# Performance work log

Measured on AMD Instinct MI355X. Metric: run time of the kernel, lower is better.

The kernel has to match this reference:

```python
import jax, jax.numpy as jnp
import numpy as np

B = 64        # graphs per batch
N0 = 131072   # total nodes (2048 per graph)
E = 1048576   # total edges (within-graph)
H = 128       # hidden_size
C = 7         # class_num (input feature dim)
EPS = 1e-5


def setup_inputs() -> dict:
    key = jax.random.key(0)
    ks = jax.random.split(key, 16)
    n0 = N0 // B
    x = jax.random.normal(ks[0], (N0, C), dtype=jnp.float32)
    # within-graph random edges: edge e belongs to graph e // (E//B)
    g = jnp.repeat(jnp.arange(B, dtype=jnp.int32), E // B)
    row = jax.random.randint(ks[1], (E,), 0, n0, dtype=jnp.int32) + g * n0
    col = jax.random.randint(ks[2], (E,), 0, n0, dtype=jnp.int32) + g * n0
    edge_index = jnp.stack([row, col], axis=0)
    batch = jnp.repeat(jnp.arange(B, dtype=jnp.int32), n0)
    s = 0.05
    params = dict(
        Wc1=jax.random.normal(ks[3], (C, H), jnp.float32) * s,     # conv1 weight
        Wc=jax.random.normal(ks[4], (3, H, H), jnp.float32) * s,   # conv2-4 weights
        bc=jax.random.normal(ks[5], (4, H), jnp.float32) * s,      # conv biases
        Wf=jax.random.normal(ks[6], (4, H, H), jnp.float32) * s,   # fc weights
        bf=jax.random.normal(ks[7], (4, H), jnp.float32) * s,      # fc biases
        bn_g=jnp.ones((4, H), jnp.float32),                        # BN gamma
        bn_b=jnp.zeros((4, H), jnp.float32),                       # BN beta
        Ws1=jax.random.normal(ks[8], (4, H, 1), jnp.float32) * s,  # SAG GraphConv root weight
        Ws2=jax.random.normal(ks[9], (4, H, 1), jnp.float32) * s,  # SAG GraphConv neighbor weight
        bs=jax.random.normal(ks[10], (4, 1), jnp.float32) * s,     # SAG GraphConv bias
    )
    return dict(x=x, edge_index=edge_index, batch=batch, **params)


def _gcn_conv(x, W, b, row, col, m, N):
    # PyG GCNConv with self loops: out_i = sum_{j->i} h_j / sqrt(d_i d_j) + h_i / d_i + b
    h = x @ W
    deg = jax.ops.segment_sum(m, col, num_segments=N) + 1.0  # +1 for self loop
    dis = jax.lax.rsqrt(deg)
    norm = dis[row] * dis[col] * m  # masked-out edges contribute 0
    agg = jax.ops.segment_sum(h[row] * norm[:, None], col, num_segments=N)
    return agg + h * (dis * dis)[:, None] + b


def _sag_score(x, W1, W2, b, row, col, m, N):
    # GraphConv(H, 1, aggr='add'): score_i = W1^T x_i + W2^T sum_{j->i} x_j + b
    nbr = jax.ops.segment_sum(x[row] * m[:, None], col, num_segments=N)
    return (x @ W1 + nbr @ W2 + b).reshape(-1)


def _bn(x, g, b):
    mu = jnp.mean(x, axis=0)
    var = jnp.mean((x - mu) ** 2, axis=0)  # biased, matches torch BN training
    return (x - mu) * jax.lax.rsqrt(var + EPS) * g + b


def reference(x, edge_index, batch, Wc1, Wc, bc, Wf, bf, bn_g, bn_b, Ws1, Ws2, bs):
    row, col = edge_index[0], edge_index[1]
    m = jnp.ones(row.shape, x.dtype)  # edge validity mask (static-size edge list)
    n = x.shape[0] // B               # nodes per graph (equal-size graphs)
    for i in range(4):
        N = B * n
        W = Wc1 if i == 0 else Wc[i - 1]
        h = _gcn_conv(x, W, bc[i], row, col, m, N)
        h = jax.nn.relu(h @ Wf[i] + bf[i])
        h = _bn(h, bn_g[i], bn_b[i])
        # SAGPooling(ratio=0.5): per-graph top-k by GraphConv score, x *= tanh(score)
        score = _sag_score(h, Ws1[i], Ws2[i], bs[i], row, col, m, N)
        k = n // 2
        _, idx = jax.lax.top_k(score.reshape(B, n), k)  # [B, k] per-graph indices
        perm = (idx + jnp.arange(B, dtype=idx.dtype)[:, None] * n).reshape(-1)
        x = h[perm] * jnp.tanh(score[perm])[:, None]
        # re-index edges; mask edges touching removed nodes
        inv = jnp.full((N,), -1, dtype=row.dtype).at[perm].set(
            jnp.arange(B * k, dtype=row.dtype))
        nr, nc = inv[row], inv[col]
        valid = (nr >= 0) & (nc >= 0)
        m = m * valid.astype(m.dtype)
        row = jnp.where(valid, nr, 0)
        col = jnp.where(valid, nc, 0)
        n = k
    # global_mean_pool over block-structured batch -> [B, H]
    return x.reshape(B, n, -1).mean(axis=1)
```

## Files before the change

### kernel.cpp

```cpp
#include <hip/hip_runtime.h>
#include <cstdint>

#define HB 128
#define NB 64
#define NE 1048576
#define EG (NE / 256)

typedef float v2f __attribute__((ext_vector_type(2)));

__global__ __launch_bounds__(256) void init_edges_k(const int* __restrict__ ei,
    int* __restrict__ row, int* __restrict__ col, int* __restrict__ gcnt0,
    int* __restrict__ ecnt0, int E) {
  int e = blockIdx.x * blockDim.x + threadIdx.x;
  if (e < E) { row[e] = ei[e]; col[e] = ei[E + e]; }
  if (blockIdx.x == 0) {
    if (threadIdx.x < NB) gcnt0[threadIdx.x] = E / NB;
    if (threadIdx.x == 0) *ecnt0 = E;
  }
}

__global__ __launch_bounds__(256) void conv_fc0_k(const float* __restrict__ aggx,
    const float* __restrict__ Wc1, const float* __restrict__ bc0,
    const float* __restrict__ Wf, const float* __restrict__ bf0,
    float* __restrict__ out, int N, float* __restrict__ stat) {
  __shared__ float lt[64][128];
  __shared__ float laggx[64][8];
  __shared__ float lwc1[7 * 128];
  float2 (*red)[128] = (float2(*)[128])lt;
  int tid = threadIdx.x;
  int tx = tid & 31, ty = tid >> 5;
  long rowbase = (long)blockIdx.x * 64;
  for (int i = tid; i < 7 * 32; i += 256)
    ((float4*)lwc1)[i] = ((const float4*)Wc1)[i];
  if (tid < 128) {
    int lr = tid >> 1, lq = (tid & 1) * 4;
    *(float4*)&laggx[lr][lq] = *(const float4*)(aggx + (rowbase + lr) * 8 + lq);
  }
  __syncthreads();
  float4 tacc[8];
  float4 bcv = ((const float4*)bc0)[tx];
  #pragma unroll
  for (int r = 0; r < 8; ++r) tacc[r] = bcv;
  #pragma unroll
  for (int k = 0; k < 7; ++k) {
    float4 wv = ((float4*)lwc1)[k * 32 + tx];
    #pragma unroll
    for (int r = 0; r < 8; ++r) {
      float xv = laggx[ty + 8 * r][k];
      tacc[r].x += xv * wv.x; tacc[r].y += xv * wv.y;
      tacc[r].z += xv * wv.z; tacc[r].w += xv * wv.w;
    }
  }
  #pragma unroll
  for (int r = 0; r < 8; ++r)
    *(float4*)&lt[ty + 8 * r][4 * tx] = tacc[r];
  __syncthreads();
  v2f acc2[16];
  #pragma unroll
  for (int r = 0; r < 16; ++r) acc2[r] = (v2f){0.f, 0.f};
  for (int kc = 0; kc < 16; ++kc) {
    float4 wreg[8];
    #pragma unroll
    for (int k = 0; k < 8; ++k)
      wreg[k] = *(const float4*)(Wf + (size_t)(kc * 8 + k) * HB + 4 * tx);
    #pragma unroll
    for (int kk = 0; kk < 8; kk += 4) {
      float4 xreg[8];
      #pragma unroll
      for (int r = 0; r < 8; ++r)
        xreg[r] = *(const float4*)&lt[ty + 8 * r][kc * 8 + kk];
      #pragma unroll
      for (int k2 = 0; k2 < 4; ++k2) {
        float4 wv = wreg[kk + k2];
        v2f wlo = {wv.x, wv.y}, whi = {wv.z, wv.w};
        #pragma unroll
        for (int r = 0; r < 8; ++r) {
          float xv = ((const float*)&xreg[r])[k2];
          v2f xvv = {xv, xv};
          acc2[2 * r]     += xvv * wlo;
          acc2[2 * r + 1] += xvv * whi;
        }
      }
    }
  }
  float4 bv = ((const float4*)bf0)[tx];
  float4 psum = make_float4(0.f, 0.f, 0.f, 0.f);
  float4 psq  = make_float4(0.f, 0.f, 0.f, 0.f);
  __syncthreads();
  #pragma unroll
  for (int r = 0; r < 8; ++r) {
    float4 v;
    v.x = fmaxf(acc2[2 * r].x + bv.x, 0.f);
    v.y = fmaxf(acc2[2 * r].y + bv.y, 0.f);
    v.z = fmaxf(acc2[2 * r + 1].x + bv.z, 0.f);
    v.w = fmaxf(acc2[2 * r + 1].y + bv.w, 0.f);
    psum.x += v.x; psum.y += v.y; psum.z += v.z; psum.w += v.w;
    psq.x += v.x * v.x; psq.y += v.y * v.y;
    psq.z += v.z * v.z; psq.w += v.w * v.w;
    *(float4*)(out + (size_t)(rowbase + ty + 8 * r) * HB + 4 * tx) = v;
  }
  red[ty][4 * tx + 0] = make_float2(psum.x, psq.x);
  red[ty][4 * tx + 1] = make_float2(psum.y, psq.y);
  red[ty][4 * tx + 2] = make_float2(psum.z, psq.z);
  red[ty][4 * tx + 3] = make_float2(psum.w, psq.w);
  __syncthreads();
  if (tid < 128) {
    float s = 0.f, q = 0.f;
    #pragma unroll
    for (int t = 0; t < 8; ++t) { s += red[t][tid].x; q += red[t][tid].y; }
    float* st = stat + ((blockIdx.x & 7) << 8);
    atomicAdd(&st[tid], s);
    atomicAdd(&st[128 + tid], q);
  }
}

__global__ __launch_bounds__(256) void gemm128_k(const float* __restrict__ X,
    const float* __restrict__ W, const float* __restrict__ bias,
    float* __restrict__ out, int N, int flags,
    const int* __restrict__ sel, const float* __restrict__ scale,
    const float* __restrict__ bnsc, float* __restrict__ stat) {
  __shared__ float2 red[8][128];
  float (*Xs)[64][8] = (float(*)[64][8])red;
  int tid = threadIdx.x;
  int tx = tid & 31;
  int ty = tid >> 5;
  long bb = blockIdx.x;
  bool gmode = (flags & 4) != 0;
  if (gmode) {
    long cpx = gridDim.x >> 3;
    bb = (bb & 7) * cpx + (bb >> 3);
  }
  long rowbase = bb * 64;
  v2f acc2[16];
  #pragma unroll
  for (int r = 0; r < 16; ++r) acc2[r] = (v2f){0.f, 0.f};
  int lr = tid >> 1, lq = (tid & 1) * 4;
  const float* xrow = nullptr;
  float lsc = 1.f;
  if (tid < 128) {
    long srcrow = rowbase + lr;
    if (gmode) { srcrow = sel[rowbase + lr]; lsc = scale[rowbase + lr]; }
    xrow = X + (size_t)srcrow * HB + lq;
  }
  auto loadx = [&](int kc) -> float4 {
    float4 v = *(const float4*)(xrow + kc * 8);
    if (gmode) {
      int ch = kc * 8 + lq;
      float4 a = *(const float4*)(bnsc + ch);
      float4 b = *(const float4*)(bnsc + 128 + ch);
      v.x = (v.x * a.x + b.x) * lsc; v.y = (v.y * a.y + b.y) * lsc;
      v.z = (v.z * a.z + b.z) * lsc; v.w = (v.w * a.w + b.w) * lsc;
    }
    return v;
  };
  if (tid < 128) *(float4*)&Xs[0][lr][lq] = loadx(0);
  __syncthreads();
  for (int kc = 0; kc < 16; ++kc) {
    int cur = kc & 1;
    if (kc < 15 && tid < 128)
      *(float4*)&Xs[cur ^ 1][lr][lq] = loadx(kc + 1);
    float4 wreg[8];
    #pragma unroll
    for (int k = 0; k < 8; ++k)
      wreg[k] = *(const float4*)(W + (size_t)(kc * 8 + k) * HB + 4 * tx);
    #pragma unroll
    for (int kk = 0; kk < 8; kk += 4) {
      float4 xreg[8];
      #pragma unroll
      for (int r = 0; r < 8; ++r)
        xreg[r] = *(const float4*)&Xs[cur][ty + 8 * r][kk];
      #pragma unroll
      for (int k = 0; k < 4; ++k) {
        float4 wv = wreg[kk + k];
        v2f wlo = {wv.x, wv.y}, whi = {wv.z, wv.w};
        #pragma unroll
        for (int r = 0; r < 8; ++r) {
          float xv = ((const float*)&xreg[r])[k];
          v2f xvv = {xv, xv};
          acc2[2 * r]     += xvv * wlo;
          acc2[2 * r + 1] += xvv * whi;
        }
      }
    }
    __syncthreads();
  }
  float4 bv = make_float4(0.f, 0.f, 0.f, 0.f);
  if (flags & 1) bv = ((const float4*)bias)[tx];
  float4 psum = make_float4(0.f, 0.f, 0.f, 0.f);
  float4 psq  = make_float4(0.f, 0.f, 0.f, 0.f);
  #pragma unroll
  for (int r = 0; r < 8; ++r) {
    float4 v;
    v.x = acc2[2 * r].x + bv.x;     v.y = acc2[2 * r].y + bv.y;
    v.z = acc2[2 * r + 1].x + bv.z; v.w = acc2[2 * r + 1].y + bv.w;
    if (flags & 2) {
      v.x = fmaxf(v.x, 0.f); v.y = fmaxf(v.y, 0.f);
      v.z = fmaxf(v.z, 0.f); v.w = fmaxf(v.w, 0.f);
    }
    if (flags & 8) {
      psum.x += v.x; psum.y += v.y; psum.z += v.z; psum.w += v.w;
      psq.x += v.x * v.x; psq.y += v.y * v.y;
      psq.z += v.z * v.z; psq.w += v.w * v.w;
    }
    *(float4*)(out + (size_t)(rowbase + ty + 8 * r) * HB + 4 * tx) = v;
  }
  if (flags & 8) {
    red[ty][4 * tx + 0] = make_float2(psum.x, psq.x);
    red[ty][4 * tx + 1] = make_float2(psum.y, psq.y);
    red[ty][4 * tx + 2] = make_float2(psum.z, psq.z);
    red[ty][4 * tx + 3] = make_float2(psum.w, psq.w);
    __syncthreads();
    if (tid < 128) {
      float s = 0.f, q = 0.f;
      #pragma unroll
      for (int t = 0; t < 8; ++t) { s += red[t][tid].x; q += red[t][tid].y; }
      float* st = stat + ((blockIdx.x & 7) << 8);
      atomicAdd(&st[tid], s);
      atomicAdd(&st[128 + tid], q);
    }
  }
}

__global__ __launch_bounds__(1024) void csr_build_k(const int* __restrict__ row,
    const int* __restrict__ col, const int* __restrict__ gcnt,
    float* __restrict__ dis, int* __restrict__ off, int* __restrict__ srow,
    float* __restrict__ snorm, int n) {
  extern __shared__ int lds[];
  int* ldeg = lds;
  int* lsa  = lds + n;
  int* lsb  = lds + 2 * n;
  float* ldis = (float*)(lds + 3 * n);
  __shared__ int e01[2];
  int g = blockIdx.x, tid = threadIdx.x;
  if (tid == 0) {
    int s = 0;
    for (int gg = 0; gg < g; ++gg) s += gcnt[gg];
    e01[0] = s; e01[1] = s + gcnt[g];
  }
  int base = g * n;
  for (int i = tid; i < n; i += 1024) ldeg[i] = 0;
  __syncthreads();
  int e0 = e01[0], e1 = e01[1];
  for (int e = e0 + tid; e < e1; e += 1024) atomicAdd(&ldeg[col[e] - base], 1);
  __syncthreads();
  for (int i = tid; i < n; i += 1024) {
    int d = ldeg[i];
    ldis[i] = rsqrtf((float)d + 1.f);
    lsa[i] = d;
  }
  __syncthreads();
  int* src = lsa; int* dst = lsb;
  for (int o = 1; o < n; o <<= 1) {
    for (int i = tid; i < n; i += 1024) dst[i] = src[i] + ((i >= o) ? src[i - o] : 0);
    __syncthreads();
    int* t = src; src = dst; dst = t;
  }
  for (int i = tid; i < n; i += 1024) {
    int d = ldeg[i];
    int ex = src[i] - d;
    off[base + i] = e0 + ex;
    ldeg[i] = ex;
    dis[base + i] = ldis[i];
  }
  if (tid == 0) off[base + n] = e1;
  __syncthreads();
  for (int e = e0 + tid; e < e1; e += 1024) {
    int r = row[e], c = col[e];
    int lc = c - base;
    int p = e0 + atomicAdd(&ldeg[lc], 1);
    srow[p] = r;
    snorm[p] = ldis[r - base] * ldis[lc];
  }
}

__global__ __launch_bounds__(256) void agg7_k(const float* __restrict__ x,
    const int* __restrict__ srow, const float* __restrict__ snorm,
    const int* __restrict__ off, const float* __restrict__ dis,
    float* __restrict__ aggx, int N) {
  int cpx = gridDim.x >> 3;
  int b = blockIdx.x;
  int bid = (b & 7) * cpx + (b >> 3);
  int gid = bid * 256 + threadIdx.x;
  int node = gid >> 3, c = gid & 7;
  if (node >= N) return;
  float acc = 0.f;
  if (c < 7) {
    int s = off[node], e = off[node + 1];
    for (int j = s; j < e; ++j) acc += x[(size_t)srow[j] * 7 + c] * snorm[j];
    float d = dis[node];
    acc += x[(size_t)node * 7 + c] * d * d;
  }
  aggx[(size_t)node * 8 + c] = acc;
}

__global__ __launch_bounds__(256) void gather_combine_k(const float* __restrict__ hw,
    const int* __restrict__ srow, const float* __restrict__ snorm,
    const int* __restrict__ off, const float* __restrict__ dis,
    const float* __restrict__ bc, float* __restrict__ out, int N) {
  int cpx = gridDim.x >> 3;
  int b = blockIdx.x;
  int bid = (b & 7) * cpx + (b >> 3);
  int gid = bid * 256 + threadIdx.x;
  int node = gid >> 5;
  if (node >= N) return;
  int ch = (gid & 31) * 4;
  int s = off[node], e = off[node + 1];
  float4 acc = make_float4(0.f, 0.f, 0.f, 0.f);
  for (int j = s; j < e; ++j) {
    int r = srow[j];
    float nm = snorm[j];
    float4 v = *(const float4*)(hw + (size_t)r * HB + ch);
    acc.x += v.x * nm; acc.y += v.y * nm; acc.z += v.z * nm; acc.w += v.w * nm;
  }
  float d = dis[node], d2 = d * d;
  float4 h = *(const float4*)(hw + (size_t)node * HB + ch);
  float4 b4 = *(const float4*)(bc + ch);
  acc.x += h.x * d2 + b4.x; acc.y += h.y * d2 + b4.y;
  acc.z += h.z * d2 + b4.z; acc.w += h.w * d2 + b4.w;
  *(float4*)(out + (size_t)node * HB + ch) = acc;
}

__global__ __launch_bounds__(128) void bnfin_k(const float* __restrict__ stat8,
    const float* __restrict__ g, const float* __restrict__ b,
    float* __restrict__ sc, int N) {
  int c = threadIdx.x;
  if (c < 128) {
    float s = 0.f, q = 0.f;
    #pragma unroll
    for (int sh = 0; sh < 8; ++sh) {
      s += stat8[sh * 256 + c];
      q += stat8[sh * 256 + 128 + c];
    }
    float mu = s / N;
    float var = q / N - mu * mu;
    float a = g[c] * rsqrtf(var + 1e-5f);
    sc[c] = a;
    sc[128 + c] = b[c] - mu * a;
  }
}

__global__ __launch_bounds__(256) void score_prep_k(const float* __restrict__ h,
    const float* __restrict__ sc, const float* __restrict__ w1,
    const float* __restrict__ w2, float* __restrict__ selfs,
    float* __restrict__ t2, int N) {
  int gid = blockIdx.x * blockDim.x + threadIdx.x;
  int node = gid >> 6;
  if (node >= N) return;
  int lane = gid & 63, c = lane * 2;
  float2 v = *(const float2*)(h + (size_t)node * HB + c);
  v.x = v.x * sc[c] + sc[128 + c];
  v.y = v.y * sc[c + 1] + sc[128 + c + 1];
  float s1 = v.x * w1[c] + v.y * w1[c + 1];
  float s2 = v.x * w2[c] + v.y * w2[c + 1];
  #pragma unroll
  for (int off = 32; off > 0; off >>= 1) {
    s1 += __shfl_xor(s1, off);
    s2 += __shfl_xor(s2, off);
  }
  if (lane == 0) { selfs[node] = s1; t2[node] = s2; }
}

__global__ __launch_bounds__(256) void score_k(const float* __restrict__ selfs,
    const float* __restrict__ t2, const int* __restrict__ srow,
    const int* __restrict__ off, const float* __restrict__ bs,
    float* __restrict__ score, int N) {
  int i = blockIdx.x * blockDim.x + threadIdx.x;
  if (i >= N) return;
  float s = selfs[i] + bs[0];
  int e0 = off[i], e1 = off[i + 1];
  for (int j = e0; j < e1; ++j) s += t2[srow[j]];
  score[i] = s;
}

__global__ __launch_bounds__(256) void rank_topk_k(const float* __restrict__ score,
    int* __restrict__ inv, int* __restrict__ sel, float* __restrict__ scale,
    int n, int k, int bpg) {
  extern __shared__ float ls[];
  int g = blockIdx.x / bpg, sub = blockIdx.x % bpg;
  int tid = threadIdx.x;
  const float* sg = score + (size_t)g * n;
  for (int i = tid; i < n; i += 256) ls[i] = sg[i];
  __syncthreads();
  int i0 = sub * 256 + tid;
  float s0 = ls[i0];
  int r0 = 0;
  for (int jb = 0; jb < n; jb += 4) {
    float4 v = *(const float4*)(ls + jb);
    r0 += (v.x > s0) || (v.x == s0 && (jb + 0) < i0);
    r0 += (v.y > s0) || (v.y == s0 && (jb + 1) < i0);
    r0 += (v.z > s0) || (v.z == s0 && (jb + 2) < i0);
    r0 += (v.w > s0) || (v.w == s0 && (jb + 3) < i0);
  }
  if (r0 < k) {
    inv[(size_t)g * n + i0] = g * k + r0;
    sel[(size_t)g * k + r0] = g * n + i0;
    scale[(size_t)g * k + r0] = tanhf(s0);
  } else inv[(size_t)g * n + i0] = -1;
}

__global__ __launch_bounds__(256) void gather_x_k(const float* __restrict__ h,
    const float* __restrict__ bnsc, const int* __restrict__ sel,
    const float* __restrict__ scale, float* __restrict__ xout, int M) {
  int gid = blockIdx.x * blockDim.x + threadIdx.x;
  int r = gid >> 5;
  if (r >= M) return;
  int ch = (gid & 31) * 4;
  int old = sel[r];
  float sc = scale[r];
  float4 v = *(const float4*)(h + (size_t)old * HB + ch);
  float4 a = *(const float4*)(bnsc + ch);
  float4 b = *(const float4*)(bnsc + 128 + ch);
  v.x = (v.x * a.x + b.x) * sc; v.y = (v.y * a.y + b.y) * sc;
  v.z = (v.z * a.z + b.z) * sc; v.w = (v.w * a.w + b.w) * sc;
  *(float4*)(xout + (size_t)r * HB + ch) = v;
}

__global__ __launch_bounds__(256) void cmpA_k(const int* __restrict__ row,
    const int* __restrict__ col, const int* __restrict__ inv,
    const int* __restrict__ ecnt, int* __restrict__ bcnt) {
  int e = blockIdx.x * 256 + threadIdx.x;
  bool valid = false;
  if (e < *ecnt) {
    int nr = inv[row[e]], nc = inv[col[e]];
    valid = (nr >= 0) && (nc >= 0);
  }
  unsigned long long mask = __ballot(valid);
  __shared__ int ws[4];
  int lane = threadIdx.x & 63, wid = threadIdx.x >> 6;
  if (lane == 0) ws[wid] = __popcll(mask);
  __syncthreads();
  if (threadIdx.x == 0) bcnt[blockIdx.x] = ws[0] + ws[1] + ws[2] + ws[3];
}

__global__ __launch_bounds__(1024) void cmpB_k(const int* __restrict__ bcnt,
    int* __restrict__ bbase, int* __restrict__ total) {
  __shared__ int s[1024];
  int tid = threadIdx.x;
  int v0 = bcnt[4 * tid], v1 = bcnt[4 * tid + 1];
  int v2 = bcnt[4 * tid + 2], v3 = bcnt[4 * tid + 3];
  int tsum = v0 + v1 + v2 + v3;
  s[tid] = tsum; __syncthreads();
  for (int o = 1; o < 1024; o <<= 1) {
    int t = (tid >= o) ? s[tid - o] : 0;
    __syncthreads();
    s[tid] += t;
    __syncthreads();
  }
  int base = s[tid] - tsum;
  bbase[4 * tid] = base;
  bbase[4 * tid + 1] = base + v0;
  bbase[4 * tid + 2] = base + v0 + v1;
  bbase[4 * tid + 3] = base + v0 + v1 + v2;
  if (tid == 1023) *total = s[1023];
}

__global__ __launch_bounds__(256) void cmpC_k(const int* __restrict__ row,
    const int* __restrict__ col, const int* __restrict__ inv,
    const int* __restrict__ ecnt, const int* __restrict__ bbase,
    int* __restrict__ nrow, int* __restrict__ ncol, int* __restrict__ gcnt,
    int khalf) {
  int e = blockIdx.x * 256 + threadIdx.x;
  bool valid = false; int nr = 0, nc = 0;
  if (e < *ecnt) {
    nr = inv[row[e]]; nc = inv[col[e]];
    valid = (nr >= 0) && (nc >= 0);
  }
  unsigned long long mask = __ballot(valid);
  int lane = threadIdx.x & 63, wid = threadIdx.x >> 6;
  __shared__ int ws[4];
  __shared__ int lg[NB];
  if (threadIdx.x < NB) lg[threadIdx.x] = 0;
  if (lane == 0) ws[wid] = __popcll(mask);
  __syncthreads();
  if (threadIdx.x == 0) {
    int a = ws[0], b = ws[1], c2 = ws[2];
    ws[0] = 0; ws[1] = a; ws[2] = a + b; ws[3] = a + b + c2;
  }
  __syncthreads();
  if (valid) {
    unsigned long long lt = ((unsigned long long)1 << lane) - 1;
    int pos = bbase[blockIdx.x] + ws[wid] + (int)__popcll(mask & lt);
    nrow[pos] = nr;
    ncol[pos] = nc;
    atomicAdd(&lg[nc / khalf], 1);
  }
  __syncthreads();
  if (threadIdx.x < NB && lg[threadIdx.x]) atomicAdd(&gcnt[threadIdx.x], lg[threadIdx.x]);
}

__global__ __launch_bounds__(128) void pool_k(const float* __restrict__ x,
    float* __restrict__ out, int n) {
  int g = blockIdx.x, c = threadIdx.x;
  float s = 0.f;
  for (int r = 0; r < n; ++r) s += x[((size_t)g * n + r) * HB + c];
  out[g * HB + c] = s / n;
}

extern "C" void kernel_launch(void* const* d_in, const int* in_sizes, int n_in,
                              void* d_out, int out_size, void* d_ws, size_t ws_size,
                              hipStream_t stream) {
  const float* x_in = (const float*)d_in[0];
  const int*   ei   = (const int*)d_in[1];
  const float* Wc1  = (const float*)d_in[3];
  const float* Wc   = (const float*)d_in[4];
  const float* bc   = (const float*)d_in[5];
  const float* Wf   = (const float*)d_in[6];
  const float* bf   = (const float*)d_in[7];
  const float* bng  = (const float*)d_in[8];
  const float* bnb  = (const float*)d_in[9];
  const float* Ws1  = (const float*)d_in[10];
  const float* Ws2  = (const float*)d_in[11];
  const float* bs   = (const float*)d_in[12];

  const int N0 = 131072, E = NE;
  char* p = (char*)d_ws;
  auto alloc = [&](size_t bytes) -> char* {
    char* r = p; p += (bytes + 255) & ~(size_t)255; return r;
  };
  float* A    = (float*)alloc((size_t)N0 * HB * 4);
  float* Bb   = (float*)alloc((size_t)N0 * HB * 4);
  float* Cc   = (float*)alloc((size_t)(N0 / 2) * HB * 4);
  float* aggx = (float*)alloc((size_t)N0 * 8 * 4);
  int*   rowA = (int*)alloc((size_t)E * 4);
  int*   colA = (int*)alloc((size_t)E * 4);
  int*   rowB = (int*)alloc((size_t)E * 4);
  int*   colB = (int*)alloc((size_t)E * 4);
  float* dis  = (float*)alloc((size_t)N0 * 4);
  float* selfs= (float*)alloc((size_t)N0 * 4);
  float* t2v  = (float*)alloc((size_t)N0 * 4);
  float* score= (float*)alloc((size_t)N0 * 4);
  int*   inv  = (int*)alloc((size_t)N0 * 4);
  int*   off  = (int*)alloc((size_t)(N0 + 1) * 4);
  int*   sel  = (int*)alloc((size_t)(N0 / 2) * 4);
  float* scale= (float*)alloc((size_t)(N0 / 2) * 4);
  int*   bcnt = (int*)alloc((size_t)EG * 4);
  int*   bbase= (int*)alloc((size_t)EG * 4);
  int*   gcntL= (int*)alloc(4 * NB * 4);
  float* stat8= (float*)alloc(4 * 8 * 256 * 4);
  float* bnsc = (float*)alloc(256 * 4);
  int*   ecnt = (int*)alloc(2 * 4);

  hipMemsetAsync(stat8, 0, 4 * 8 * 256 * 4, stream);
  hipMemsetAsync(gcntL, 0, 4 * NB * 4, stream);

  init_edges_k<<<E / 256, 256, 0, stream>>>(ei, rowA, colA, gcntL, ecnt, E);

  int* rowCur = rowA; int* colCur = colA;
  int* rowNxt = rowB; int* colNxt = colB;
  int* ecntCur = ecnt; int* ecntNxt = ecnt + 1;

  int n = 2048;
  for (int i = 0; i < 4; ++i) {
    int N = NB * n, khalf = n >> 1;
    float* statL = stat8 + (size_t)i * 8 * 256;
    int*   srow  = rowNxt;
    float* snorm = (float*)colNxt;
    csr_build_k<<<NB, 1024, (size_t)16 * n, stream>>>(
        rowCur, colCur, gcntL + i * NB, dis, off, srow, snorm, n);
    if (i == 0) {
      agg7_k<<<N / 32, 256, 0, stream>>>(x_in, srow, snorm, off, dis, aggx, N);
      conv_fc0_k<<<N / 64, 256, 0, stream>>>(aggx, Wc1, bc, Wf, bf, A, N, statL);
    } else {
      const float* W = Wc + (size_t)(i - 1) * HB * HB;
      gemm128_k<<<N / 64, 256, 0, stream>>>(A, W, nullptr, Cc, N, 4,
                                            sel, scale, bnsc, nullptr);
      gather_combine_k<<<N / 8, 256, 0, stream>>>(Cc, srow, snorm, off, dis,
                                                  bc + (size_t)i * HB, Bb, N);
      gemm128_k<<<N / 64, 256, 0, stream>>>(
          Bb, Wf + (size_t)i * HB * HB, bf + (size_t)i * HB, A, N, 1 | 2 | 8,
          nullptr, nullptr, nullptr, statL);
    }
    bnfin_k<<<1, 128, 0, stream>>>(statL, bng + (size_t)i * HB, bnb + (size_t)i * HB, bnsc, N);
    score_prep_k<<<N / 4, 256, 0, stream>>>(
        A, bnsc, Ws1 + (size_t)i * HB, Ws2 + (size_t)i * HB, selfs, t2v, N);
    score_k<<<(N + 255) / 256, 256, 0, stream>>>(selfs, t2v, srow, off, bs + i, score, N);
    int bpg = n / 256;
    rank_topk_k<<<NB * bpg, 256, (size_t)n * 4, stream>>>(
        score, inv, sel, scale, n, khalf, bpg);
    if (i < 3) {
      cmpA_k<<<EG, 256, 0, stream>>>(rowCur, colCur, inv, ecntCur, bcnt);
      cmpB_k<<<1, 1024, 0, stream>>>(bcnt, bbase, ecntNxt);
      cmpC_k<<<EG, 256, 0, stream>>>(rowCur, colCur, inv, ecntCur, bbase,
                                     rowNxt, colNxt, gcntL + (i + 1) * NB, khalf);
      int* t;
      t = rowCur; rowCur = rowNxt; rowNxt = t;
      t = colCur; colCur = colNxt; colNxt = t;
      t = ecntCur; ecntCur = ecntNxt; ecntNxt = t;
    } else {
      gather_x_k<<<(NB * khalf) / 8, 256, 0, stream>>>(
          A, bnsc, sel, scale, Cc, NB * khalf);
    }
    n = khalf;
  }
  pool_k<<<NB, 128, 0, stream>>>(Cc, (float*)d_out, n);
}
```

Measured before the change: 630.4 us.

## Fuse aggregate-first GCN conv and fc GEMMs into one kernel per layer

Layers 1-3 now run one kernel instead of three. Each block first gathers the neighbour-aggregated, BN-normalised and tanh-scaled input rows into LDS, doing aggregation before the conv weight, which is valid by linearity. It then runs the conv GEMM and the fc GEMM back to back from LDS, adding bias, ReLU and BN statistics at the end. This removes two intermediate 128-wide HBM round trips and two launches. In exchange the gather is now per 128-channel row, repeated on source nodes with selection and affine work, and uses 64 KB of LDS per block, which lowers occupancy. Input and output buffers alternate between layers to avoid aliasing.

Result: faster. 595.1 us (-5.6%).

```diff
diff --git a/kernel.cpp b/kernel.cpp
--- a/kernel.cpp
+++ b/kernel.cpp
@@ -114,110 +114,163 @@
   }
 }
 
-__global__ __launch_bounds__(256) void gemm128_k(const float* __restrict__ X,
-    const float* __restrict__ W, const float* __restrict__ bias,
-    float* __restrict__ out, int N, int flags,
-    const int* __restrict__ sel, const float* __restrict__ scale,
-    const float* __restrict__ bnsc, float* __restrict__ stat) {
-  __shared__ float2 red[8][128];
-  float (*Xs)[64][8] = (float(*)[64][8])red;
+__global__ __launch_bounds__(256) void conv_fc_k(const float* __restrict__ Ap,
+    const float* __restrict__ bnsc, const int* __restrict__ sel,
+    const float* __restrict__ scale, const int* __restrict__ srow,
+    const float* __restrict__ snorm, const int* __restrict__ off,
+    const float* __restrict__ dis, const float* __restrict__ Wc,
+    const float* __restrict__ bc0, const float* __restrict__ Wf,
+    const float* __restrict__ bf0, float* __restrict__ out, int N,
+    float* __restrict__ stat) {
+  __shared__ float xag[64][128];
+  __shared__ float lt[64][128];
+  float2 (*red)[128] = (float2(*)[128])lt;
   int tid = threadIdx.x;
-  int tx = tid & 31;
-  int ty = tid >> 5;
-  long bb = blockIdx.x;
-  bool gmode = (flags & 4) != 0;
-  if (gmode) {
-    long cpx = gridDim.x >> 3;
-    bb = (bb & 7) * cpx + (bb >> 3);
-  }
+  int tx = tid & 31, ty = tid >> 5;
+  long cpx = gridDim.x >> 3;
+  long bb = ((long)blockIdx.x & 7) * cpx + ((long)blockIdx.x >> 3);
   long rowbase = bb * 64;
+  {
+    int r = tid >> 2;
+    int chq = (tid & 3) * 32;
+    int node = rowbase + r;
+    float4 av[8], bv8[8];
+    #pragma unroll
+    for (int q = 0; q < 8; ++q) {
+      av[q]  = *(const float4*)(bnsc + chq + 4 * q);
+      bv8[q] = *(const float4*)(bnsc + 128 + chq + 4 * q);
+    }
+    int e0 = off[node], e1 = off[node + 1];
+    float dv = dis[node];
+    float4 acc[8];
+    {
+      float sc = scale[node] * dv * dv;
+      const float* xr = Ap + (size_t)sel[node] * HB + chq;
+      #pragma unroll
+      for (int q = 0; q < 8; ++q) {
+        float4 v = *(const float4*)(xr + 4 * q);
+        acc[q].x = (v.x * av[q].x + bv8[q].x) * sc;
+        acc[q].y = (v.y * av[q].y + bv8[q].y) * sc;
+        acc[q].z = (v.z * av[q].z + bv8[q].z) * sc;
+        acc[q].w = (v.w * av[q].w + bv8[q].w) * sc;
+      }
+    }
+    for (int j = e0; j < e1; ++j) {
+      int srcn = srow[j];
+      float sc = snorm[j] * scale[srcn];
+      const float* xr = Ap + (size_t)sel[srcn] * HB + chq;
+      #pragma unroll
+      for (int q = 0; q < 8; ++q) {
+        float4 v = *(const float4*)(xr + 4 * q);
+        acc[q].x += (v.x * av[q].x + bv8[q].x) * sc;
+        acc[q].y += (v.y * av[q].y + bv8[q].y) * sc;
+        acc[q].z += (v.z * av[q].z + bv8[q].z) * sc;
+        acc[q].w += (v.w * av[q].w + bv8[q].w) * sc;
+      }
+    }
+    #pragma unroll
+    for (int q = 0; q < 8; ++q) *(float4*)&xag[r][chq + 4 * q] = acc[q];
+  }
+  __syncthreads();
+  {
+    float4 bcv = ((const float4*)bc0)[tx];
+    v2f acc2[16];
+    #pragma unroll
+    for (int r = 0; r < 8; ++r) {
+      acc2[2 * r]     = (v2f){bcv.x, bcv.y};
+      acc2[2 * r + 1] = (v2f){bcv.z, bcv.w};
+    }
+    for (int kc = 0; kc < 16; ++kc) {
+      float4 wreg[8];
+      #pragma unroll
+      for (int k = 0; k < 8; ++k)
+        wreg[k] = *(const float4*)(Wc + (size_t)(kc * 8 + k) * HB + 4 * tx);
+      #pragma unroll
+      for (int kk = 0; kk < 8; kk += 4) {
+        float4 xreg[8];
+        #pragma unroll
+        for (int r = 0; r < 8; ++r)
+          xreg[r] = *(const float4*)&xag[ty + 8 * r][kc * 8 + kk];
+        #pragma unroll
+        for (int k2 = 0; k2 < 4; ++k2) {
+          float4 wv = wreg[kk + k2];
+          v2f wlo = {wv.x, wv.y}, whi = {wv.z, wv.w};
+          #pragma unroll
+          for (int r = 0; r < 8; ++r) {
+            float xv = ((const float*)&xreg[r])[k2];
+            v2f xvv = {xv, xv};
+            acc2[2 * r]     += xvv * wlo;
+            acc2[2 * r + 1] += xvv * whi;
+          }
+        }
+      }
+    }
+    __syncthreads();
+    #pragma unroll
+    for (int r = 0; r < 8; ++r) {
+      float4 v;
+      v.x = acc2[2 * r].x;     v.y = acc2[2 * r].y;
+      v.z = acc2[2 * r + 1].x; v.w = acc2[2 * r + 1].y;
+      *(float4*)&lt[ty + 8 * r][4 * tx] = v;
+    }
+  }
+  __syncthreads();
   v2f acc2[16];
   #pragma unroll
   for (int r = 0; r < 16; ++r) acc2[r] = (v2f){0.f, 0.f};
-  int lr = tid >> 1, lq = (tid & 1) * 4;
-  const float* xrow = nullptr;
-  float lsc = 1.f;
-  if (tid < 128) {
-    long srcrow = rowbase + lr;
-    if (gmode) { srcrow = sel[rowbase + lr]; lsc = scale[rowbase + lr]; }
-    xrow = X + (size_t)srcrow * HB + lq;
-  }
-  auto loadx = [&](int kc) -> float4 {
-    float4 v = *(const float4*)(xrow + kc * 8);
-    if (gmode) {
-      int ch = kc * 8 + lq;
-      float4 a = *(const float4*)(bnsc + ch);
-      float4 b = *(const float4*)(bnsc + 128 + ch);
-      v.x = (v.x * a.x + b.x) * lsc; v.y = (v.y * a.y + b.y) * lsc;
-      v.z = (v.z * a.z + b.z) * lsc; v.w = (v.w * a.w + b.w) * lsc;
-    }
-    return v;
-  };
-  if (tid < 128) *(float4*)&Xs[0][lr][lq] = loadx(0);
-  __syncthreads();
   for (int kc = 0; kc < 16; ++kc) {
-    int cur = kc & 1;
-    if (kc < 15 && tid < 128)
-      *(float4*)&Xs[cur ^ 1][lr][lq] = loadx(kc + 1);
     float4 wreg[8];
     #pragma unroll
     for (int k = 0; k < 8; ++k)
-      wreg[k] = *(const float4*)(W + (size_t)(kc * 8 + k) * HB + 4 * tx);
+      wreg[k] = *(const float4*)(Wf + (size_t)(kc * 8 + k) * HB + 4 * tx);
     #pragma unroll
     for (int kk = 0; kk < 8; kk += 4) {
       float4 xreg[8];
       #pragma unroll
       for (int r = 0; r < 8; ++r)
-        xreg[r] = *(const float4*)&Xs[cur][ty + 8 * r][kk];
-      #pragma unroll
-      for (int k = 0; k < 4; ++k) {
-        float4 wv = wreg[kk + k];
+        xreg[r] = *(const float4*)&lt[ty + 8 * r][kc * 8 + kk];
+      #pragma unroll
+      for (int k2 = 0; k2 < 4; ++k2) {
+        float4 wv = wreg[kk + k2];
         v2f wlo = {wv.x, wv.y}, whi = {wv.z, wv.w};
         #pragma unroll
         for (int r = 0; r < 8; ++r) {
-          float xv = ((const float*)&xreg[r])[k];
+          float xv = ((const float*)&xreg[r])[k2];
           v2f xvv = {xv, xv};
           acc2[2 * r]     += xvv * wlo;
           acc2[2 * r + 1] += xvv * whi;
         }
       }
     }
-    __syncthreads();
-  }
-  float4 bv = make_float4(0.f, 0.f, 0.f, 0.f);
-  if (flags & 1) bv = ((const float4*)bias)[tx];
+  }
+  float4 bv = ((const float4*)bf0)[tx];
   float4 psum = make_float4(0.f, 0.f, 0.f, 0.f);
   float4 psq  = make_float4(0.f, 0.f, 0.f, 0.f);
+  __syncthreads();
   #pragma unroll
   for (int r = 0; r < 8; ++r) {
     float4 v;
-    v.x = acc2[2 * r].x + bv.x;     v.y = acc2[2 * r].y + bv.y;
-    v.z = acc2[2 * r + 1].x + bv.z; v.w = acc2[2 * r + 1].y + bv.w;
-    if (flags & 2) {
-      v.x = fmaxf(v.x, 0.f); v.y = fmaxf(v.y, 0.f);
-      v.z = fmaxf(v.z, 0.f); v.w = fmaxf(v.w, 0.f);
-    }
-    if (flags & 8) {
-      psum.x += v.x; psum.y += v.y; psum.z += v.z; psum.w += v.w;
-      psq.x += v.x * v.x; psq.y += v.y * v.y;
-      psq.z += v.z * v.z; psq.w += v.w * v.w;
-    }
+    v.x = fmaxf(acc2[2 * r].x + bv.x, 0.f);
+    v.y = fmaxf(acc2[2 * r].y + bv.y, 0.f);
+    v.z = fmaxf(acc2[2 * r + 1].x + bv.z, 0.f);
+    v.w = fmaxf(acc2[2 * r + 1].y + bv.w, 0.f);
+    psum.x += v.x; psum.y += v.y; psum.z += v.z; psum.w += v.w;
+    psq.x += v.x * v.x; psq.y += v.y * v.y;
+    psq.z += v.z * v.z; psq.w += v.w * v.w;
     *(float4*)(out + (size_t)(rowbase + ty + 8 * r) * HB + 4 * tx) = v;
   }
-  if (flags & 8) {
-    red[ty][4 * tx + 0] = make_float2(psum.x, psq.x);
-    red[ty][4 * tx + 1] = make_float2(psum.y, psq.y);
-    red[ty][4 * tx + 2] = make_float2(psum.z, psq.z);
-    red[ty][4 * tx + 3] = make_float2(psum.w, psq.w);
-    __syncthreads();
-    if (tid < 128) {
-      float s = 0.f, q = 0.f;
-      #pragma unroll
-      for (int t = 0; t < 8; ++t) { s += red[t][tid].x; q += red[t][tid].y; }
-      float* st = stat + ((blockIdx.x & 7) << 8);
-      atomicAdd(&st[tid], s);
-      atomicAdd(&st[128 + tid], q);
-    }
+  red[ty][4 * tx + 0] = make_float2(psum.x, psq.x);
+  red[ty][4 * tx + 1] = make_float2(psum.y, psq.y);
+  red[ty][4 * tx + 2] = make_float2(psum.z, psq.z);
+  red[ty][4 * tx + 3] = make_float2(psum.w, psq.w);
+  __syncthreads();
+  if (tid < 128) {
+    float s = 0.f, q = 0.f;
+    #pragma unroll
+    for (int t = 0; t < 8; ++t) { s += red[t][tid].x; q += red[t][tid].y; }
+    float* st = stat + (((int)blockIdx.x & 7) << 8);
+    atomicAdd(&st[tid], s);
+    atomicAdd(&st[128 + tid], q);
   }
 }
 
@@ -291,33 +344,6 @@
     acc += x[(size_t)node * 7 + c] * d * d;
   }
   aggx[(size_t)node * 8 + c] = acc;
-}
-
-__global__ __launch_bounds__(256) void gather_combine_k(const float* __restrict__ hw,
-    const int* __restrict__ srow, const float* __restrict__ snorm,
-    const int* __restrict__ off, const float* __restrict__ dis,
-    const float* __restrict__ bc, float* __restrict__ out, int N) {
-  int cpx = gridDim.x >> 3;
-  int b = blockIdx.x;
-  int bid = (b & 7) * cpx + (b >> 3);
-  int gid = bid * 256 + threadIdx.x;
-  int node = gid >> 5;
-  if (node >= N) return;
-  int ch = (gid & 31) * 4;
-  int s = off[node], e = off[node + 1];
-  float4 acc = make_float4(0.f, 0.f, 0.f, 0.f);
-  for (int j = s; j < e; ++j) {
-    int r = srow[j];
-    float nm = snorm[j];
-    float4 v = *(const float4*)(hw + (size_t)r * HB + ch);
-    acc.x += v.x * nm; acc.y += v.y * nm; acc.z += v.z * nm; acc.w += v.w * nm;
-  }
-  float d = dis[node], d2 = d * d;
-  float4 h = *(const float4*)(hw + (size_t)node * HB + ch);
-  float4 b4 = *(const float4*)(bc + ch);
-  acc.x += h.x * d2 + b4.x; acc.y += h.y * d2 + b4.y;
-  acc.z += h.z * d2 + b4.z; acc.w += h.w * d2 + b4.w;
-  *(float4*)(out + (size_t)node * HB + ch) = acc;
 }
 
 __global__ __launch_bounds__(128) void bnfin_k(const float* __restrict__ stat8,
@@ -553,26 +579,24 @@
   for (int i = 0; i < 4; ++i) {
     int N = NB * n, khalf = n >> 1;
     float* statL = stat8 + (size_t)i * 8 * 256;
+    const float* Xin  = (i == 2) ? Bb : A;
+    float*       Xout = (i == 0 || i == 2) ? A : Bb;
     int*   srow  = rowNxt;
     float* snorm = (float*)colNxt;
     csr_build_k<<<NB, 1024, (size_t)16 * n, stream>>>(
         rowCur, colCur, gcntL + i * NB, dis, off, srow, snorm, n);
     if (i == 0) {
       agg7_k<<<N / 32, 256, 0, stream>>>(x_in, srow, snorm, off, dis, aggx, N);
-      conv_fc0_k<<<N / 64, 256, 0, stream>>>(aggx, Wc1, bc, Wf, bf, A, N, statL);
+      conv_fc0_k<<<N / 64, 256, 0, stream>>>(aggx, Wc1, bc, Wf, bf, Xout, N, statL);
     } else {
-      const float* W = Wc + (size_t)(i - 1) * HB * HB;
-      gemm128_k<<<N / 64, 256, 0, stream>>>(A, W, nullptr, Cc, N, 4,
-                                            sel, scale, bnsc, nullptr);
-      gather_combine_k<<<N / 8, 256, 0, stream>>>(Cc, srow, snorm, off, dis,
-                                                  bc + (size_t)i * HB, Bb, N);
-      gemm128_k<<<N / 64, 256, 0, stream>>>(
-          Bb, Wf + (size_t)i * HB * HB, bf + (size_t)i * HB, A, N, 1 | 2 | 8,
-          nullptr, nullptr, nullptr, statL);
+      conv_fc_k<<<N / 64, 256, 0, stream>>>(
+          Xin, bnsc, sel, scale, srow, snorm, off, dis,
+          Wc + (size_t)(i - 1) * HB * HB, bc + (size_t)i * HB,
+          Wf + (size_t)i * HB * HB, bf + (size_t)i * HB, Xout, N, statL);
     }
     bnfin_k<<<1, 128, 0, stream>>>(statL, bng + (size_t)i * HB, bnb + (size_t)i * HB, bnsc, N);
     score_prep_k<<<N / 4, 256, 0, stream>>>(
-        A, bnsc, Ws1 + (size_t)i * HB, Ws2 + (size_t)i * HB, selfs, t2v, N);
+        Xout, bnsc, Ws1 + (size_t)i * HB, Ws2 + (size_t)i * HB, selfs, t2v, N);
     score_k<<<(N + 255) / 256, 256, 0, stream>>>(selfs, t2v, srow, off, bs + i, score, N);
     int bpg = n / 256;
     rank_topk_k<<<NB * bpg, 256, (size_t)n * 4, stream>>>(
@@ -588,7 +612,7 @@
       t = ecntCur; ecntCur = ecntNxt; ecntNxt = t;
     } else {
       gather_x_k<<<(NB * khalf) / 8, 256, 0, stream>>>(
-          A, bnsc, sel, scale, Cc, NB * khalf);
+          Xout, bnsc, sel, scale, Cc, NB * khalf);
     }
     n = khalf;
   }
```
